# Kernel optimization log

Hardware: AMD Instinct MI355X
Metric: run time of the kernel (lower is better)

The kernel has to match this reference:

```python
import jax, jax.numpy as jnp
import numpy as np

N = 100000      # nodes
E = 1600000     # edges (avg degree 16)
IN, HID, OUT = 128, 64, 64


def setup_inputs() -> dict:
    key = jax.random.key(0)
    ks = jax.random.split(key, 8)
    s = 0.05
    return {
        "x": jax.random.normal(ks[0], (N, IN), jnp.float32),
        "edge_index": jax.random.randint(ks[1], (2, E), 0, N, dtype=jnp.int32),
        "W1": jax.random.normal(ks[2], (IN, HID), jnp.float32) * s,
        "b1": jnp.zeros((HID,), jnp.float32),
        "W2": jax.random.normal(ks[3], (HID, HID), jnp.float32) * s,
        "b2": jnp.zeros((HID,), jnp.float32),
        "W3": jax.random.normal(ks[4], (HID, OUT), jnp.float32) * s,
        "b3": jnp.zeros((OUT,), jnp.float32),
    }


def reference(x, edge_index, W1, b1, W2, b2, W3, b3):
    src, dst = edge_index[0], edge_index[1]

    def gcn_conv(h, W, b):
        # GCNConv(normalize=False): dense linear, gather source features,
        # scatter-add into target nodes, add bias.
        m = (h @ W)[src]                                   # [E, F_out]
        return jax.ops.segment_sum(m, dst, num_segments=N) + b

    h = jax.nn.relu(gcn_conv(x, W1, b1))   # dropout: identity (eval mode)
    h = jax.nn.relu(gcn_conv(h, W2, b2))
    return jax.nn.sigmoid(gcn_conv(h, W3, b3))
```

## Files before the change

### kernel.cpp

```cpp
#include <hip/hip_runtime.h>


#define FOUT 64
#define NPB2 196
#define NBUCKET 511
#define CAP 4096
#define CHUNK 8192

__device__ __forceinline__ unsigned short f2bf(float f) {
    unsigned u = __float_as_uint(f);
    u += 0x7FFF + ((u >> 16) & 1);
    return (unsigned short)(u >> 16);
}
__device__ __forceinline__ float bf2f(unsigned short b) {
    return __uint_as_float(((unsigned)b) << 16);
}

template<int K>
__global__ __launch_bounds__(256) void k_linear(
    const float* __restrict__ in, const float* __restrict__ W,
    unsigned short* __restrict__ outbf, int n) {
    constexpr int XSTR = (K == 128) ? 132 : 68;
    __shared__ float4 sW4[K * 16];
    __shared__ float xs[64 * XSTR];

    const int t = threadIdx.x;
    const int base = blockIdx.x * 64;

    const float4* W4 = (const float4*)W;
#pragma unroll
    for (int i = 0; i < K * 16 / 256; ++i) sW4[t + i * 256] = W4[t + i * 256];

    constexpr int CPR = K / 4;
#pragma unroll
    for (int i = 0; i < 64 * CPR / 256; ++i) {
        int flat = t + i * 256;
        int row = flat / CPR;
        int c4 = flat % CPR;
        int rg = base + row;
        if (rg < n) {
            float4 v = *(const float4*)(in + (size_t)rg * K + c4 * 4);
            *(float4*)&xs[row * XSTR + c4 * 4] = v;
        }
    }
    __syncthreads();

    const int fq = t & 15;
    const int slot = (t >> 4) & 3;
    const int wave = t >> 6;
    const int r0 = wave * 16 + slot * 4;

    float4 acc[4];
#pragma unroll
    for (int i = 0; i < 4; ++i) acc[i] = make_float4(0.f, 0.f, 0.f, 0.f);

#pragma unroll 8
    for (int k = 0; k < K; k += 4) {
        float4 w0 = sW4[(k + 0) * 16 + fq];
        float4 w1 = sW4[(k + 1) * 16 + fq];
        float4 w2 = sW4[(k + 2) * 16 + fq];
        float4 w3 = sW4[(k + 3) * 16 + fq];
#pragma unroll
        for (int i = 0; i < 4; ++i) {
            float4 xv = *(const float4*)&xs[(r0 + i) * XSTR + k];
            acc[i].x = fmaf(xv.x, w0.x, acc[i].x);
            acc[i].y = fmaf(xv.x, w0.y, acc[i].y);
            acc[i].z = fmaf(xv.x, w0.z, acc[i].z);
            acc[i].w = fmaf(xv.x, w0.w, acc[i].w);
            acc[i].x = fmaf(xv.y, w1.x, acc[i].x);
            acc[i].y = fmaf(xv.y, w1.y, acc[i].y);
            acc[i].z = fmaf(xv.y, w1.z, acc[i].z);
            acc[i].w = fmaf(xv.y, w1.w, acc[i].w);
            acc[i].x = fmaf(xv.z, w2.x, acc[i].x);
            acc[i].y = fmaf(xv.z, w2.y, acc[i].y);
            acc[i].z = fmaf(xv.z, w2.z, acc[i].z);
            acc[i].w = fmaf(xv.z, w2.w, acc[i].w);
            acc[i].x = fmaf(xv.w, w3.x, acc[i].x);
            acc[i].y = fmaf(xv.w, w3.y, acc[i].y);
            acc[i].z = fmaf(xv.w, w3.z, acc[i].z);
            acc[i].w = fmaf(xv.w, w3.w, acc[i].w);
        }
    }

#pragma unroll
    for (int i = 0; i < 4; ++i) {
        int rg = base + r0 + i;
        if (rg < n) {
            ushort4 us;
            us.x = f2bf(acc[i].x); us.y = f2bf(acc[i].y);
            us.z = f2bf(acc[i].z); us.w = f2bf(acc[i].w);
            *(ushort4*)(outbf + (size_t)rg * FOUT + fq * 4) = us;
        }
    }
}

__global__ __launch_bounds__(512) void k_init(int* __restrict__ gcursor) {
    gcursor[threadIdx.x] = threadIdx.x * CAP;
}

__global__ __launch_bounds__(256) void k_bin(
    const int* __restrict__ src, const int* __restrict__ dst,
    int* __restrict__ gcursor, int* __restrict__ bins, int ne) {
    __shared__ int cnt[NBUCKET];
    __shared__ int gbase[NBUCKET];

    const int t = threadIdx.x;
    const int cbeg = blockIdx.x * CHUNK;
    const int cend = min(cbeg + CHUNK, ne);

    for (int i = t; i < NBUCKET; i += 256) cnt[i] = 0;
    __syncthreads();

    for (int e = cbeg + t; e < cend; e += 256)
        atomicAdd(&cnt[dst[e] / NPB2], 1);
    __syncthreads();

    for (int i = t; i < NBUCKET; i += 256) {
        int c = cnt[i];
        gbase[i] = (c > 0) ? atomicAdd(&gcursor[i], c) : 0;
    }
    __syncthreads();
    for (int i = t; i < NBUCKET; i += 256) cnt[i] = 0;
    __syncthreads();

    for (int e = cbeg + t; e < cend; e += 256) {
        int d = dst[e];
        int b = d / NPB2;
        int dl = d - b * NPB2;
        int lpos = atomicAdd(&cnt[b], 1);
        int gpos = gbase[b] + lpos;
        if (gpos < (b + 1) * CAP)
            bins[gpos] = src[e] | (dl << 17);
    }
}

__global__ __launch_bounds__(512) void k_bscan(
    const int* __restrict__ gcursor, int* __restrict__ bucket_base) {
    __shared__ int s[512];
    const int t = threadIdx.x;
    int c = 0;
    if (t < NBUCKET) c = min(gcursor[t] - t * CAP, CAP);
    s[t] = c;
    __syncthreads();
    for (int ofs = 1; ofs < 512; ofs <<= 1) {
        int v = (t >= ofs) ? s[t - ofs] : 0;
        __syncthreads();
        s[t] += v;
        __syncthreads();
    }
    if (t < NBUCKET) bucket_base[t] = s[t] - c;
}

__global__ __launch_bounds__(256) void k_csr(
    const int* __restrict__ gcursor, const int* __restrict__ bins,
    const int* __restrict__ bucket_base, int* __restrict__ row_ofs,
    int* __restrict__ csr_src, int n) {
    __shared__ int recs[CAP];
    __shared__ int cnt[NPB2];
    __shared__ int ofs[NPB2];
    __shared__ int cur[NPB2];
    __shared__ int sscan[256];

    const int t = threadIdx.x;
    const int b = blockIdx.x;
    const int c = min(gcursor[b] - b * CAP, CAP);
    const int baseg = bucket_base[b];

    for (int i = t; i < c; i += 256) recs[i] = bins[b * CAP + i];
    for (int i = t; i < NPB2; i += 256) cnt[i] = 0;
    __syncthreads();

    for (int i = t; i < c; i += 256)
        atomicAdd(&cnt[((unsigned)recs[i]) >> 17], 1);
    __syncthreads();

    int v = (t < NPB2) ? cnt[t] : 0;
    sscan[t] = v;
    __syncthreads();
    for (int o = 1; o < 256; o <<= 1) {
        int u = (t >= o) ? sscan[t - o] : 0;
        __syncthreads();
        sscan[t] += u;
        __syncthreads();
    }
    if (t < NPB2) {
        ofs[t] = sscan[t] - v;
        cur[t] = sscan[t] - v;
        int node = b * NPB2 + t;
        if (node <= n) row_ofs[node] = baseg + ofs[t];
    }
    __syncthreads();

    for (int i = t; i < c; i += 256) {
        unsigned r = (unsigned)recs[i];
        int dl = r >> 17;
        int p = atomicAdd(&cur[dl], 1);
        csr_src[baseg + p] = (int)(r & 0x1FFFF);
    }
}

template<int ACT>
__global__ __launch_bounds__(256) void k_agg(
    const int* __restrict__ row_ofs, const int* __restrict__ csr_src,
    const unsigned short* __restrict__ msg, const float* __restrict__ bias,
    float* __restrict__ out, int n) {
    const int node = blockIdx.x * 4 + (threadIdx.x >> 6);
    if (node >= n) return;
    const int lane = threadIdx.x & 63;
    const int beg = row_ofs[node];
    const int end = row_ofs[node + 1];
    float acc = 0.f;
    int j = beg;
    for (; j + 4 <= end; j += 4) {
        int s0 = csr_src[j];
        int s1 = csr_src[j + 1];
        int s2 = csr_src[j + 2];
        int s3 = csr_src[j + 3];
        float v0 = bf2f(msg[(size_t)s0 * FOUT + lane]);
        float v1 = bf2f(msg[(size_t)s1 * FOUT + lane]);
        float v2 = bf2f(msg[(size_t)s2 * FOUT + lane]);
        float v3 = bf2f(msg[(size_t)s3 * FOUT + lane]);
        acc += (v0 + v1) + (v2 + v3);
    }
    for (; j < end; ++j)
        acc += bf2f(msg[(size_t)csr_src[j] * FOUT + lane]);
    float v = acc + bias[lane];
    out[(size_t)node * FOUT + lane] =
        (ACT == 0) ? fmaxf(v, 0.f) : 1.f / (1.f + __expf(-v));
}

extern "C" void kernel_launch(void* const* d_in, const int* in_sizes, int n_in,
                              void* d_out, int out_size, void* d_ws, size_t ws_size,
                              hipStream_t stream) {
    const float* x  = (const float*)d_in[0];
    const int*   ei = (const int*)d_in[1];
    const float* W1 = (const float*)d_in[2];
    const float* b1 = (const float*)d_in[3];
    const float* W2 = (const float*)d_in[4];
    const float* b2 = (const float*)d_in[5];
    const float* W3 = (const float*)d_in[6];
    const float* b3 = (const float*)d_in[7];
    float* out = (float*)d_out;

    const int n  = in_sizes[0] / 128;
    const int ne = in_sizes[1] / 2;
    const int* src = ei;
    const int* dst = ei + ne;

    const size_t feat_elems = (size_t)n * FOUT;

    unsigned short* msg16 = (unsigned short*)d_ws;
    float* B        = (float*)(msg16 + feat_elems);
    int*   bins     = (int*)(B + feat_elems);
    int*   gcursor  = bins + (size_t)NBUCKET * CAP;
    int*   bucket_base = gcursor + 512;
    int*   row_ofs  = bucket_base + 512;
    int*   csr_src  = row_ofs + n + 1;

    const int gLin = (n + 63) / 64;
    const int gBin = (ne + CHUNK - 1) / CHUNK;
    const int gAgg = (n + 3) / 4;

    k_init<<<1, NBUCKET, 0, stream>>>(gcursor);
    k_bin<<<gBin, 256, 0, stream>>>(src, dst, gcursor, bins, ne);
    k_bscan<<<1, 512, 0, stream>>>(gcursor, bucket_base);
    k_csr<<<NBUCKET, 256, 0, stream>>>(gcursor, bins, bucket_base, row_ofs, csr_src, n);

    k_linear<128><<<gLin, 256, 0, stream>>>(x, W1, msg16, n);
    k_agg<0><<<gAgg, 256, 0, stream>>>(row_ofs, csr_src, msg16, b1, B, n);
    k_linear<64><<<gLin, 256, 0, stream>>>(B, W2, msg16, n);
    k_agg<0><<<gAgg, 256, 0, stream>>>(row_ofs, csr_src, msg16, b2, B, n);
    k_linear<64><<<gLin, 256, 0, stream>>>(B, W3, msg16, n);
    k_agg<1><<<gAgg, 256, 0, stream>>>(row_ofs, csr_src, msg16, b3, out, n);
}
```

Before: 403.8 us.

## Store hidden activations in bf16 and aggregate two edges per wave with packed loads

The intermediate hidden activations between layers are now written as bf16 instead of fp32, and the next linear kernel reads bf16 and expands it when loading into shared memory. This halves that intermediate traffic. The aggregation kernel now has each half-wave handle a different edge, loading packed 32-bit bf16 pairs, then combines the halves with a cross-lane shuffle. That doubles the edges in flight per wave and widens each load. The cost is extra rounding of the hidden activations and a shuffle reduction step.

```diff
diff --git a/kernel.cpp b/kernel.cpp
--- a/kernel.cpp
+++ b/kernel.cpp
@@ -12,13 +12,16 @@
     u += 0x7FFF + ((u >> 16) & 1);
     return (unsigned short)(u >> 16);
 }
-__device__ __forceinline__ float bf2f(unsigned short b) {
-    return __uint_as_float(((unsigned)b) << 16);
-}
-
-template<int K>
+__device__ __forceinline__ float bflo(unsigned u) {
+    return __uint_as_float(u << 16);
+}
+__device__ __forceinline__ float bfhi(unsigned u) {
+    return __uint_as_float(u & 0xFFFF0000u);
+}
+
+template<int K, int INBF>
 __global__ __launch_bounds__(256) void k_linear(
-    const float* __restrict__ in, const float* __restrict__ W,
+    const void* __restrict__ inv, const float* __restrict__ W,
     unsigned short* __restrict__ outbf, int n) {
     constexpr int XSTR = (K == 128) ? 132 : 68;
     __shared__ float4 sW4[K * 16];
@@ -31,16 +34,40 @@
 #pragma unroll
     for (int i = 0; i < K * 16 / 256; ++i) sW4[t + i * 256] = W4[t + i * 256];
 
-    constexpr int CPR = K / 4;
-#pragma unroll
-    for (int i = 0; i < 64 * CPR / 256; ++i) {
-        int flat = t + i * 256;
-        int row = flat / CPR;
-        int c4 = flat % CPR;
-        int rg = base + row;
-        if (rg < n) {
-            float4 v = *(const float4*)(in + (size_t)rg * K + c4 * 4);
-            *(float4*)&xs[row * XSTR + c4 * 4] = v;
+    if (INBF) {
+        const unsigned short* in16 = (const unsigned short*)inv;
+        constexpr int QPR = K / 8;
+#pragma unroll
+        for (int i = 0; i < 64 * QPR / 256; ++i) {
+            int flat = t + i * 256;
+            int row = flat / QPR;
+            int q = flat % QPR;
+            int rg = base + row;
+            if (rg < n) {
+                uint4 u = *(const uint4*)(in16 + (size_t)rg * K + q * 8);
+                float* xp = &xs[row * XSTR + q * 8];
+                float4 a, b;
+                a.x = bflo(u.x); a.y = bfhi(u.x);
+                a.z = bflo(u.y); a.w = bfhi(u.y);
+                b.x = bflo(u.z); b.y = bfhi(u.z);
+                b.z = bflo(u.w); b.w = bfhi(u.w);
+                *(float4*)(xp) = a;
+                *(float4*)(xp + 4) = b;
+            }
+        }
+    } else {
+        const float* in = (const float*)inv;
+        constexpr int CPR = K / 4;
+#pragma unroll
+        for (int i = 0; i < 64 * CPR / 256; ++i) {
+            int flat = t + i * 256;
+            int row = flat / CPR;
+            int c4 = flat % CPR;
+            int rg = base + row;
+            if (rg < n) {
+                float4 v = *(const float4*)(in + (size_t)rg * K + c4 * 4);
+                *(float4*)&xs[row * XSTR + c4 * 4] = v;
+            }
         }
     }
     __syncthreads();
@@ -157,7 +184,6 @@
     int* __restrict__ csr_src, int n) {
     __shared__ int recs[CAP];
     __shared__ int cnt[NPB2];
-    __shared__ int ofs[NPB2];
     __shared__ int cur[NPB2];
     __shared__ int sscan[256];
 
@@ -184,10 +210,9 @@
         __syncthreads();
     }
     if (t < NPB2) {
-        ofs[t] = sscan[t] - v;
         cur[t] = sscan[t] - v;
         int node = b * NPB2 + t;
-        if (node <= n) row_ofs[node] = baseg + ofs[t];
+        if (node <= n) row_ofs[node] = baseg + sscan[t] - v;
     }
     __syncthreads();
 
@@ -199,34 +224,62 @@
     }
 }
 
-template<int ACT>
+template<int ACT, int OUTBF>
 __global__ __launch_bounds__(256) void k_agg(
     const int* __restrict__ row_ofs, const int* __restrict__ csr_src,
-    const unsigned short* __restrict__ msg, const float* __restrict__ bias,
-    float* __restrict__ out, int n) {
+    const unsigned* __restrict__ msg32, const float* __restrict__ bias,
+    void* __restrict__ outv, int n) {
     const int node = blockIdx.x * 4 + (threadIdx.x >> 6);
     if (node >= n) return;
     const int lane = threadIdx.x & 63;
+    const int half = lane >> 5;
+    const int p = lane & 31;
     const int beg = row_ofs[node];
     const int end = row_ofs[node + 1];
-    float acc = 0.f;
+
+    float a0 = 0.f, a1 = 0.f;
     int j = beg;
-    for (; j + 4 <= end; j += 4) {
-        int s0 = csr_src[j];
-        int s1 = csr_src[j + 1];
-        int s2 = csr_src[j + 2];
-        int s3 = csr_src[j + 3];
-        float v0 = bf2f(msg[(size_t)s0 * FOUT + lane]);
-        float v1 = bf2f(msg[(size_t)s1 * FOUT + lane]);
-        float v2 = bf2f(msg[(size_t)s2 * FOUT + lane]);
-        float v3 = bf2f(msg[(size_t)s3 * FOUT + lane]);
-        acc += (v0 + v1) + (v2 + v3);
-    }
-    for (; j < end; ++j)
-        acc += bf2f(msg[(size_t)csr_src[j] * FOUT + lane]);
-    float v = acc + bias[lane];
-    out[(size_t)node * FOUT + lane] =
-        (ACT == 0) ? fmaxf(v, 0.f) : 1.f / (1.f + __expf(-v));
+    for (; j + 8 <= end; j += 8) {
+        int sA = csr_src[j + 0 + half];
+        int sB = csr_src[j + 2 + half];
+        int sC = csr_src[j + 4 + half];
+        int sD = csr_src[j + 6 + half];
+        unsigned vA = msg32[(size_t)sA * 32 + p];
+        unsigned vB = msg32[(size_t)sB * 32 + p];
+        unsigned vC = msg32[(size_t)sC * 32 + p];
+        unsigned vD = msg32[(size_t)sD * 32 + p];
+        a0 += bflo(vA) + bflo(vB) + bflo(vC) + bflo(vD);
+        a1 += bfhi(vA) + bfhi(vB) + bfhi(vC) + bfhi(vD);
+    }
+    for (; j < end; j += 2) {
+        if (j + half < end) {
+            int s = csr_src[j + half];
+            unsigned v = msg32[(size_t)s * 32 + p];
+            a0 += bflo(v);
+            a1 += bfhi(v);
+        }
+    }
+    a0 += __shfl_xor(a0, 32);
+    a1 += __shfl_xor(a1, 32);
+
+    if (half == 0) {
+        float v0 = a0 + bias[2 * p];
+        float v1 = a1 + bias[2 * p + 1];
+        if (ACT == 0) {
+            v0 = fmaxf(v0, 0.f);
+            v1 = fmaxf(v1, 0.f);
+        } else {
+            v0 = 1.f / (1.f + __expf(-v0));
+            v1 = 1.f / (1.f + __expf(-v1));
+        }
+        if (OUTBF) {
+            ushort2 us; us.x = f2bf(v0); us.y = f2bf(v1);
+            *(ushort2*)((unsigned short*)outv + (size_t)node * FOUT + 2 * p) = us;
+        } else {
+            float2 f2; f2.x = v0; f2.y = v1;
+            *(float2*)((float*)outv + (size_t)node * FOUT + 2 * p) = f2;
+        }
+    }
 }
 
 extern "C" void kernel_launch(void* const* d_in, const int* in_sizes, int n_in,
@@ -250,8 +303,8 @@
     const size_t feat_elems = (size_t)n * FOUT;
 
     unsigned short* msg16 = (unsigned short*)d_ws;
-    float* B        = (float*)(msg16 + feat_elems);
-    int*   bins     = (int*)(B + feat_elems);
+    unsigned short* B16   = msg16 + feat_elems;
+    int*   bins     = (int*)(B16 + feat_elems);
     int*   gcursor  = bins + (size_t)NBUCKET * CAP;
     int*   bucket_base = gcursor + 512;
     int*   row_ofs  = bucket_base + 512;
@@ -266,10 +319,10 @@
     k_bscan<<<1, 512, 0, stream>>>(gcursor, bucket_base);
     k_csr<<<NBUCKET, 256, 0, stream>>>(gcursor, bins, bucket_base, row_ofs, csr_src, n);
 
-    k_linear<128><<<gLin, 256, 0, stream>>>(x, W1, msg16, n);
-    k_agg<0><<<gAgg, 256, 0, stream>>>(row_ofs, csr_src, msg16, b1, B, n);
-    k_linear<64><<<gLin, 256, 0, stream>>>(B, W2, msg16, n);
-    k_agg<0><<<gAgg, 256, 0, stream>>>(row_ofs, csr_src, msg16, b2, B, n);
-    k_linear<64><<<gLin, 256, 0, stream>>>(B, W3, msg16, n);
-    k_agg<1><<<gAgg, 256, 0, stream>>>(row_ofs, csr_src, msg16, b3, out, n);
-}
+    k_linear<128, 0><<<gLin, 256, 0, stream>>>(x, W1, msg16, n);
+    k_agg<0, 1><<<gAgg, 256, 0, stream>>>(row_ofs, csr_src, (const unsigned*)msg16, b1, B16, n);
+    k_linear<64, 1><<<gLin, 256, 0, stream>>>(B16, W2, msg16, n);
+    k_agg<0, 1><<<gAgg, 256, 0, stream>>>(row_ofs, csr_src, (const unsigned*)msg16, b2, B16, n);
+    k_linear<64, 1><<<gLin, 256, 0, stream>>>(B16, W3, msg16, n);
+    k_agg<1, 0><<<gAgg, 256, 0, stream>>>(row_ofs, csr_src, (const unsigned*)msg16, b3, out, n);
+}
```

After: 376.4 us. 1.07x faster.
